# Optimization experiments

Hardware: AMD Instinct MI355X
Metric: run time of the kernel (lower is better)

Reference implementation:

```python
import jax, jax.numpy as jnp
import numpy as np

NUM_NEG = 100
TEMP = 0.05
EPS = 1e-12  # matches F.normalize eps


def _l2norm(x):
    n = jnp.sqrt(jnp.sum(x * x, axis=-1, keepdims=True))
    return x / jnp.maximum(n, EPS)


def setup_inputs() -> dict:
    key = jax.random.key(0)
    k1, k2, k3, k4, k5, k6 = jax.random.split(key, 6)
    B, S, D = 1024, 50, 64
    NUM_ITEMS = 100000  # table has NUM_ITEMS+1 rows (row 0 = padding)
    N = B * S
    return {
        "output_embeddings": jax.random.normal(k1, (B, S, D), dtype=jnp.float32),
        "target_ids": jax.random.randint(k2, (B, S), 1, NUM_ITEMS + 1, dtype=jnp.int64)
                      if jax.config.jax_enable_x64 else
                      jax.random.randint(k2, (B, S), 1, NUM_ITEMS + 1).astype(jnp.int32),
        "all_item_embeddings": jax.random.normal(k3, (NUM_ITEMS + 1, D), dtype=jnp.float32),
        "supervision_weights": jax.random.uniform(k4, (B, S), dtype=jnp.float32),
        "neg_indices": jax.random.randint(k5, (N, NUM_NEG), 1, NUM_ITEMS + 1).astype(jnp.int32),
        "alt_neg_indices": jax.random.randint(k6, (N, NUM_NEG), 1, NUM_ITEMS + 1).astype(jnp.int32),
    }


def reference(output_embeddings, target_ids, all_item_embeddings,
              supervision_weights, neg_indices, alt_neg_indices):
    B, S, D = output_embeddings.shape
    flat_out = output_embeddings.reshape(-1, D)            # [N, D]
    flat_tgt = target_ids.reshape(-1)                       # [N]
    flat_w = supervision_weights.reshape(-1)                # [N]
    valid = flat_w > 0

    vo = _l2norm(flat_out)                                  # [N, D]
    items = _l2norm(all_item_embeddings)                    # [V, D]

    pos_e = items[flat_tgt]                                 # [N, D]
    pos_logit = jnp.sum(vo * pos_e, axis=1)                 # [N]

    # resample negatives that collide with the positive target
    neg = jnp.where(neg_indices != flat_tgt[:, None], neg_indices, alt_neg_indices)
    neg_e = items[neg]                                      # [N, K, D]
    neg_logits = jnp.einsum('nd,nkd->nk', vo, neg_e)        # [N, K]

    logits = jnp.concatenate([pos_logit[:, None], neg_logits], axis=1) / TEMP
    # cross-entropy with label 0 == logsumexp - positive logit
    loss_per = jax.nn.logsumexp(logits, axis=1) - logits[:, 0]

    wm = jnp.where(valid, flat_w, 0.0)
    return jnp.sum(loss_per * wm) / jnp.sum(wm)
```

## Files before the change

kernel.cpp:

```cpp
#include <hip/hip_runtime.h>


#define D_DIM 64
#define K_NEG 100
#define INV_TEMP 20.0f
#define MAX_LOGIT 20.0f
#define LOG2E 1.4426950408889634f
#define LN2 0.6931471805599453f

#define NBLK_MAIN 2048
#define NBLK_NORM 512
#define NT 7

typedef float fv2 __attribute__((ext_vector_type(2)));

__global__ __launch_bounds__(256) void normalize_kernel(
    const float* __restrict__ items, unsigned int* __restrict__ tab, int V) {
  const int lane = threadIdx.x & 63;
  const int wid  = threadIdx.x >> 6;
  const int g = lane >> 4, q = lane & 15;
  const int waveId = blockIdx.x * 4 + wid;
  const int nWaves = gridDim.x * 4;
  for (int base = waveId * 4; base < V; base += nWaves * 4) {
    const int r = base + g;
    const bool act = (r < V);
    float4 x = make_float4(0.f, 0.f, 0.f, 0.f);
    if (act) x = *reinterpret_cast<const float4*>(items + (size_t)r * D_DIM + q * 4);
    float ss = x.x * x.x + x.y * x.y + x.z * x.z + x.w * x.w;
    ss += __shfl_xor(ss, 1);
    ss += __shfl_xor(ss, 2);
    ss += __shfl_xor(ss, 4);
    ss += __shfl_xor(ss, 8);
    const float inv = 1.0f / fmaxf(sqrtf(ss), 1e-12f);
    if (act) {
      int u = 0;
      u = __builtin_amdgcn_cvt_pk_fp8_f32(x.x * inv, x.y * inv, u, false);
      u = __builtin_amdgcn_cvt_pk_fp8_f32(x.z * inv, x.w * inv, u, true);
      tab[(size_t)r * 16 + q] = (unsigned int)u;
    }
  }
}

__global__ __launch_bounds__(256, 4) void loss_kernel(
    const float* __restrict__ oe,
    const int*   __restrict__ tgt,
    const unsigned int* __restrict__ tab,
    const float* __restrict__ wgt,
    const int*   __restrict__ negi,
    const int*   __restrict__ alti,
    float2*      __restrict__ partials,
    int N) {
  const int lane = threadIdx.x & 63;
  const int wid  = threadIdx.x >> 6;
  const int g = lane >> 2, q = lane & 3;
  const int waveId = blockIdx.x * 4 + wid;
  const int nWaves = gridDim.x * 4;

  float num = 0.f, den = 0.f;

  int row = waveId;
  float4 a0, a1, a2, a3;
  int t_r = 0;
  float w = 0.f;
  int nj0 = 0, nj1 = 0, nj2 = 0, nj3 = 0, nj4 = 0, nj5 = 0, nj6 = 0;

  if (row < N) {
    const float* orow = oe + (size_t)row * D_DIM + q * 16;
    a0 = *reinterpret_cast<const float4*>(orow + 0);
    a1 = *reinterpret_cast<const float4*>(orow + 4);
    a2 = *reinterpret_cast<const float4*>(orow + 8);
    a3 = *reinterpret_cast<const float4*>(orow + 12);
    t_r = tgt[row];
    w = wgt[row];
    const int* nrow = negi + (size_t)row * K_NEG;
    if (g >= 1) nj0 = nrow[g - 1];
    nj1 = nrow[16 + g - 1];
    nj2 = nrow[32 + g - 1];
    nj3 = nrow[48 + g - 1];
    nj4 = nrow[64 + g - 1];
    nj5 = nrow[80 + g - 1];
    if (g <= 4) nj6 = nrow[96 + g - 1];
  }

  while (row < N) {
    const int nxt = row + nWaves;
    const int* __restrict__ arow = alti + (size_t)row * K_NEG;

    int idx[NT];
    {
      int v0 = (g == 0) ? t_r : nj0;
      if (g >= 1 && v0 == t_r) v0 = arow[g - 1];
      idx[0] = v0;
      int v1 = nj1; if (v1 == t_r) v1 = arow[16 + g - 1]; idx[1] = v1;
      int v2 = nj2; if (v2 == t_r) v2 = arow[32 + g - 1]; idx[2] = v2;
      int v3 = nj3; if (v3 == t_r) v3 = arow[48 + g - 1]; idx[3] = v3;
      int v4 = nj4; if (v4 == t_r) v4 = arow[64 + g - 1]; idx[4] = v4;
      int v5 = nj5; if (v5 == t_r) v5 = arow[80 + g - 1]; idx[5] = v5;
      int v6 = 0;
      if (g <= 4) { v6 = nj6; if (v6 == t_r) v6 = arow[96 + g - 1]; }
      idx[6] = v6;
    }

    uint4 rb[NT];
#pragma unroll
    for (int t = 0; t < NT; ++t)
      rb[t] = *reinterpret_cast<const uint4*>(tab + (size_t)idx[t] * 16 + q * 4);

    float4 b0, b1, b2, b3;
    int p_t = 0; float p_w = 0.f;
    int pn0 = 0, pn1 = 0, pn2 = 0, pn3 = 0, pn4 = 0, pn5 = 0, pn6 = 0;
    b0 = b1 = b2 = b3 = make_float4(0.f, 0.f, 0.f, 0.f);
    if (nxt < N) {
      const float* prow = oe + (size_t)nxt * D_DIM + q * 16;
      b0 = *reinterpret_cast<const float4*>(prow + 0);
      b1 = *reinterpret_cast<const float4*>(prow + 4);
      b2 = *reinterpret_cast<const float4*>(prow + 8);
      b3 = *reinterpret_cast<const float4*>(prow + 12);
      p_t = tgt[nxt];
      p_w = wgt[nxt];
      const int* nrow = negi + (size_t)nxt * K_NEG;
      if (g >= 1) pn0 = nrow[g - 1];
      pn1 = nrow[16 + g - 1];
      pn2 = nrow[32 + g - 1];
      pn3 = nrow[48 + g - 1];
      pn4 = nrow[64 + g - 1];
      pn5 = nrow[80 + g - 1];
      if (g <= 4) pn6 = nrow[96 + g - 1];
    }

    const fv2 qa0 = {a0.x, a0.y}, qa1 = {a0.z, a0.w};
    const fv2 qa2 = {a1.x, a1.y}, qa3 = {a1.z, a1.w};
    const fv2 qa4 = {a2.x, a2.y}, qa5 = {a2.z, a2.w};
    const fv2 qa6 = {a3.x, a3.y}, qa7 = {a3.z, a3.w};

    fv2 ss2 = qa0 * qa0;
    ss2 += qa1 * qa1;
    ss2 += qa2 * qa2;
    ss2 += qa3 * qa3;
    ss2 += qa4 * qa4;
    ss2 += qa5 * qa5;
    ss2 += qa6 * qa6;
    ss2 += qa7 * qa7;
    float ss = ss2[0] + ss2[1];
    ss += __shfl_xor(ss, 1);
    ss += __shfl_xor(ss, 2);
    const float inv_o = 1.0f / fmaxf(sqrtf(ss), 1e-12f);

    float sumexp = 0.f;
    float pos_logit = 0.f;

#pragma unroll
    for (int t = 0; t < NT; ++t) {
      const uint4 r = rb[t];
      fv2 acc;
      acc  = qa0 * __builtin_amdgcn_cvt_pk_f32_fp8((int)r.x, false);
      acc += qa1 * __builtin_amdgcn_cvt_pk_f32_fp8((int)r.x, true);
      acc += qa2 * __builtin_amdgcn_cvt_pk_f32_fp8((int)r.y, false);
      acc += qa3 * __builtin_amdgcn_cvt_pk_f32_fp8((int)r.y, true);
      acc += qa4 * __builtin_amdgcn_cvt_pk_f32_fp8((int)r.z, false);
      acc += qa5 * __builtin_amdgcn_cvt_pk_f32_fp8((int)r.z, true);
      acc += qa6 * __builtin_amdgcn_cvt_pk_f32_fp8((int)r.w, false);
      acc += qa7 * __builtin_amdgcn_cvt_pk_f32_fp8((int)r.w, true);
      float p = acc[0] + acc[1];
      p += __shfl_xor(p, 1);
      p += __shfl_xor(p, 2);
      const int j = t * 16 + g;
      if (q == 0 && j <= K_NEG) {
        const float logit = p * inv_o * INV_TEMP;
        sumexp += exp2f((logit - MAX_LOGIT) * LOG2E);
        if (j == 0) pos_logit = logit;
      }
    }
    sumexp += __shfl_xor(sumexp, 4);
    sumexp += __shfl_xor(sumexp, 8);
    sumexp += __shfl_xor(sumexp, 16);
    sumexp += __shfl_xor(sumexp, 32);
    if (lane == 0) {
      const float lse = log2f(sumexp) * LN2 + MAX_LOGIT;
      const float loss = lse - pos_logit;
      if (w > 0.f) {
        num += loss * w;
        den += w;
      }
    }

    a0 = b0; a1 = b1; a2 = b2; a3 = b3;
    t_r = p_t; w = p_w;
    nj0 = pn0; nj1 = pn1; nj2 = pn2; nj3 = pn3; nj4 = pn4; nj5 = pn5; nj6 = pn6;
    row = nxt;
  }

  __shared__ float2 red[4];
  if (lane == 0) red[wid] = make_float2(num, den);
  __syncthreads();
  if (threadIdx.x == 0) {
    float n = 0.f, d = 0.f;
#pragma unroll
    for (int i = 0; i < 4; ++i) { n += red[i].x; d += red[i].y; }
    partials[blockIdx.x] = make_float2(n, d);
  }
}

__global__ __launch_bounds__(256) void finish_kernel(
    const float2* __restrict__ partials, int nblk, float* __restrict__ out) {
  float num = 0.f, den = 0.f;
  for (int i = threadIdx.x; i < nblk; i += 256) {
    const float2 p = partials[i];
    num += p.x;
    den += p.y;
  }
#pragma unroll
  for (int m = 1; m < 64; m <<= 1) {
    num += __shfl_xor(num, m);
    den += __shfl_xor(den, m);
  }
  __shared__ float2 red[4];
  const int wid = threadIdx.x >> 6;
  const int lane = threadIdx.x & 63;
  if (lane == 0) red[wid] = make_float2(num, den);
  __syncthreads();
  if (threadIdx.x == 0) {
    float n = 0.f, d = 0.f;
#pragma unroll
    for (int i = 0; i < 4; ++i) { n += red[i].x; d += red[i].y; }
    out[0] = n / d;
  }
}

extern "C" void kernel_launch(void* const* d_in, const int* in_sizes, int n_in,
                              void* d_out, int out_size, void* d_ws, size_t ws_size,
                              hipStream_t stream) {
  const float* oe    = (const float*)d_in[0];
  const int*   tgt   = (const int*)  d_in[1];
  const float* items = (const float*)d_in[2];
  const float* wgt   = (const float*)d_in[3];
  const int*   negi  = (const int*)  d_in[4];
  const int*   alti  = (const int*)  d_in[5];

  const int N = in_sizes[0] / D_DIM;
  const int V = in_sizes[2] / D_DIM;

  unsigned int* tab = (unsigned int*)d_ws;
  size_t off = ((size_t)V * 16 * sizeof(unsigned int) + 255) & ~(size_t)255;
  float2* partials = (float2*)((char*)d_ws + off);

  normalize_kernel<<<NBLK_NORM, 256, 0, stream>>>(items, tab, V);
  loss_kernel<<<NBLK_MAIN, 256, 0, stream>>>(oe, tgt, tab, wgt, negi, alti,
                                             partials, N);
  finish_kernel<<<1, 256, 0, stream>>>(partials, NBLK_MAIN, (float*)d_out);
}
```

Before: 70.75 us.

## Software-pipeline loss kernel with double-buffered gathers across rows

```diff
diff --git a/kernel.cpp b/kernel.cpp
--- a/kernel.cpp
+++ b/kernel.cpp
@@ -8,7 +8,7 @@
 #define LOG2E 1.4426950408889634f
 #define LN2 0.6931471805599453f
 
-#define NBLK_MAIN 2048
+#define NBLK_MAIN 1024
 #define NBLK_NORM 512
 #define NT 7
 
@@ -41,7 +41,122 @@
   }
 }
 
-__global__ __launch_bounds__(256, 4) void loss_kernel(
+
+struct Idx { int t, n0, n1, n2, n3, n4, n5, n6; };
+struct Qry { float4 a0, a1, a2, a3; float w; };
+
+__device__ __forceinline__ void load_idx(Idx& ix, const int* __restrict__ tgt,
+                                         const int* __restrict__ negi,
+                                         int row, int g) {
+  ix.t = tgt[row];
+  const int* __restrict__ nrow = negi + (size_t)row * K_NEG;
+  ix.n0 = 0;
+  ix.n6 = 0;
+  if (g >= 1) ix.n0 = nrow[g - 1];
+  ix.n1 = nrow[16 + g - 1];
+  ix.n2 = nrow[32 + g - 1];
+  ix.n3 = nrow[48 + g - 1];
+  ix.n4 = nrow[64 + g - 1];
+  ix.n5 = nrow[80 + g - 1];
+  if (g <= 4) ix.n6 = nrow[96 + g - 1];
+}
+
+__device__ __forceinline__ void load_qry(Qry& Q, const float* __restrict__ oe,
+                                         const float* __restrict__ wgt,
+                                         int row, int q) {
+  const float* __restrict__ orow = oe + (size_t)row * D_DIM + q * 16;
+  Q.a0 = *reinterpret_cast<const float4*>(orow + 0);
+  Q.a1 = *reinterpret_cast<const float4*>(orow + 4);
+  Q.a2 = *reinterpret_cast<const float4*>(orow + 8);
+  Q.a3 = *reinterpret_cast<const float4*>(orow + 12);
+  Q.w  = wgt[row];
+}
+
+__device__ __forceinline__ void resolve_gather(
+    const Idx& ix, const unsigned int* __restrict__ tab,
+    const int* __restrict__ alti, int row, int g, int q, uint4 (&rb)[NT]) {
+  const int* __restrict__ arow = alti + (size_t)row * K_NEG;
+  int id[NT];
+  {
+    int v0 = (g == 0) ? ix.t : ix.n0;
+    if (g >= 1 && v0 == ix.t) v0 = arow[g - 1];
+    id[0] = v0;
+    int v1 = ix.n1; if (v1 == ix.t) v1 = arow[16 + g - 1]; id[1] = v1;
+    int v2 = ix.n2; if (v2 == ix.t) v2 = arow[32 + g - 1]; id[2] = v2;
+    int v3 = ix.n3; if (v3 == ix.t) v3 = arow[48 + g - 1]; id[3] = v3;
+    int v4 = ix.n4; if (v4 == ix.t) v4 = arow[64 + g - 1]; id[4] = v4;
+    int v5 = ix.n5; if (v5 == ix.t) v5 = arow[80 + g - 1]; id[5] = v5;
+    int v6 = 0;
+    if (g <= 4) { v6 = ix.n6; if (v6 == ix.t) v6 = arow[96 + g - 1]; }
+    id[6] = v6;
+  }
+#pragma unroll
+  for (int t = 0; t < NT; ++t)
+    rb[t] = *reinterpret_cast<const uint4*>(tab + (size_t)id[t] * 16 + q * 4);
+}
+
+__device__ __forceinline__ void compute_row(const Qry& Q, const uint4 (&rb)[NT],
+                                            float& num, float& den,
+                                            int lane, int g, int q) {
+  const fv2 qa0 = {Q.a0.x, Q.a0.y}, qa1 = {Q.a0.z, Q.a0.w};
+  const fv2 qa2 = {Q.a1.x, Q.a1.y}, qa3 = {Q.a1.z, Q.a1.w};
+  const fv2 qa4 = {Q.a2.x, Q.a2.y}, qa5 = {Q.a2.z, Q.a2.w};
+  const fv2 qa6 = {Q.a3.x, Q.a3.y}, qa7 = {Q.a3.z, Q.a3.w};
+
+  fv2 ss2 = qa0 * qa0;
+  ss2 += qa1 * qa1;
+  ss2 += qa2 * qa2;
+  ss2 += qa3 * qa3;
+  ss2 += qa4 * qa4;
+  ss2 += qa5 * qa5;
+  ss2 += qa6 * qa6;
+  ss2 += qa7 * qa7;
+  float ss = ss2[0] + ss2[1];
+  ss += __shfl_xor(ss, 1);
+  ss += __shfl_xor(ss, 2);
+  const float inv_o = 1.0f / fmaxf(sqrtf(ss), 1e-12f);
+  const float scale = inv_o * INV_TEMP;
+
+  float sumexp = 0.f;
+  float pos_logit = 0.f;
+
+#pragma unroll
+  for (int t = 0; t < NT; ++t) {
+    const uint4 r = rb[t];
+    fv2 acc;
+    acc  = qa0 * __builtin_amdgcn_cvt_pk_f32_fp8((int)r.x, false);
+    acc += qa1 * __builtin_amdgcn_cvt_pk_f32_fp8((int)r.x, true);
+    acc += qa2 * __builtin_amdgcn_cvt_pk_f32_fp8((int)r.y, false);
+    acc += qa3 * __builtin_amdgcn_cvt_pk_f32_fp8((int)r.y, true);
+    acc += qa4 * __builtin_amdgcn_cvt_pk_f32_fp8((int)r.z, false);
+    acc += qa5 * __builtin_amdgcn_cvt_pk_f32_fp8((int)r.z, true);
+    acc += qa6 * __builtin_amdgcn_cvt_pk_f32_fp8((int)r.w, false);
+    acc += qa7 * __builtin_amdgcn_cvt_pk_f32_fp8((int)r.w, true);
+    float p = acc[0] + acc[1];
+    p += __shfl_xor(p, 1);
+    p += __shfl_xor(p, 2);
+    const int j = t * 16 + g;
+    if (q == 0 && j <= K_NEG) {
+      const float logit = p * scale;
+      sumexp += exp2f((logit - MAX_LOGIT) * LOG2E);
+      if (j == 0) pos_logit = logit;
+    }
+  }
+  sumexp += __shfl_xor(sumexp, 4);
+  sumexp += __shfl_xor(sumexp, 8);
+  sumexp += __shfl_xor(sumexp, 16);
+  sumexp += __shfl_xor(sumexp, 32);
+  if (lane == 0) {
+    const float lse = log2f(sumexp) * LN2 + MAX_LOGIT;
+    const float loss = lse - pos_logit;
+    if (Q.w > 0.f) {
+      num += loss * Q.w;
+      den += Q.w;
+    }
+  }
+}
+
+__global__ __launch_bounds__(256, 3) void loss_kernel(
     const float* __restrict__ oe,
     const int*   __restrict__ tgt,
     const unsigned int* __restrict__ tab,
@@ -59,135 +174,41 @@
   float num = 0.f, den = 0.f;
 
   int row = waveId;
-  float4 a0, a1, a2, a3;
-  int t_r = 0;
-  float w = 0.f;
-  int nj0 = 0, nj1 = 0, nj2 = 0, nj3 = 0, nj4 = 0, nj5 = 0, nj6 = 0;
+  Idx  ix;
+  Qry  qA, qB;
+  uint4 rbA[NT], rbB[NT];
 
   if (row < N) {
-    const float* orow = oe + (size_t)row * D_DIM + q * 16;
-    a0 = *reinterpret_cast<const float4*>(orow + 0);
-    a1 = *reinterpret_cast<const float4*>(orow + 4);
-    a2 = *reinterpret_cast<const float4*>(orow + 8);
-    a3 = *reinterpret_cast<const float4*>(orow + 12);
-    t_r = tgt[row];
-    w = wgt[row];
-    const int* nrow = negi + (size_t)row * K_NEG;
-    if (g >= 1) nj0 = nrow[g - 1];
-    nj1 = nrow[16 + g - 1];
-    nj2 = nrow[32 + g - 1];
-    nj3 = nrow[48 + g - 1];
-    nj4 = nrow[64 + g - 1];
-    nj5 = nrow[80 + g - 1];
-    if (g <= 4) nj6 = nrow[96 + g - 1];
+    load_idx(ix, tgt, negi, row, g);
+    load_qry(qA, oe, wgt, row, q);
+    resolve_gather(ix, tab, alti, row, g, q, rbA);
+    const int r1 = row + nWaves;
+    if (r1 < N) {
+      load_idx(ix, tgt, negi, r1, g);
+      load_qry(qB, oe, wgt, r1, q);
+    }
   }
 
   while (row < N) {
-    const int nxt = row + nWaves;
-    const int* __restrict__ arow = alti + (size_t)row * K_NEG;
-
-    int idx[NT];
     {
-      int v0 = (g == 0) ? t_r : nj0;
-      if (g >= 1 && v0 == t_r) v0 = arow[g - 1];
-      idx[0] = v0;
-      int v1 = nj1; if (v1 == t_r) v1 = arow[16 + g - 1]; idx[1] = v1;
-      int v2 = nj2; if (v2 == t_r) v2 = arow[32 + g - 1]; idx[2] = v2;
-      int v3 = nj3; if (v3 == t_r) v3 = arow[48 + g - 1]; idx[3] = v3;
-      int v4 = nj4; if (v4 == t_r) v4 = arow[64 + g - 1]; idx[4] = v4;
-      int v5 = nj5; if (v5 == t_r) v5 = arow[80 + g - 1]; idx[5] = v5;
-      int v6 = 0;
-      if (g <= 4) { v6 = nj6; if (v6 == t_r) v6 = arow[96 + g - 1]; }
-      idx[6] = v6;
-    }
-
-    uint4 rb[NT];
-#pragma unroll
-    for (int t = 0; t < NT; ++t)
-      rb[t] = *reinterpret_cast<const uint4*>(tab + (size_t)idx[t] * 16 + q * 4);
-
-    float4 b0, b1, b2, b3;
-    int p_t = 0; float p_w = 0.f;
-    int pn0 = 0, pn1 = 0, pn2 = 0, pn3 = 0, pn4 = 0, pn5 = 0, pn6 = 0;
-    b0 = b1 = b2 = b3 = make_float4(0.f, 0.f, 0.f, 0.f);
-    if (nxt < N) {
-      const float* prow = oe + (size_t)nxt * D_DIM + q * 16;
-      b0 = *reinterpret_cast<const float4*>(prow + 0);
-      b1 = *reinterpret_cast<const float4*>(prow + 4);
-      b2 = *reinterpret_cast<const float4*>(prow + 8);
-      b3 = *reinterpret_cast<const float4*>(prow + 12);
-      p_t = tgt[nxt];
-      p_w = wgt[nxt];
-      const int* nrow = negi + (size_t)nxt * K_NEG;
-      if (g >= 1) pn0 = nrow[g - 1];
-      pn1 = nrow[16 + g - 1];
-      pn2 = nrow[32 + g - 1];
-      pn3 = nrow[48 + g - 1];
-      pn4 = nrow[64 + g - 1];
-      pn5 = nrow[80 + g - 1];
-      if (g <= 4) pn6 = nrow[96 + g - 1];
-    }
-
-    const fv2 qa0 = {a0.x, a0.y}, qa1 = {a0.z, a0.w};
-    const fv2 qa2 = {a1.x, a1.y}, qa3 = {a1.z, a1.w};
-    const fv2 qa4 = {a2.x, a2.y}, qa5 = {a2.z, a2.w};
-    const fv2 qa6 = {a3.x, a3.y}, qa7 = {a3.z, a3.w};
-
-    fv2 ss2 = qa0 * qa0;
-    ss2 += qa1 * qa1;
-    ss2 += qa2 * qa2;
-    ss2 += qa3 * qa3;
-    ss2 += qa4 * qa4;
-    ss2 += qa5 * qa5;
-    ss2 += qa6 * qa6;
-    ss2 += qa7 * qa7;
-    float ss = ss2[0] + ss2[1];
-    ss += __shfl_xor(ss, 1);
-    ss += __shfl_xor(ss, 2);
-    const float inv_o = 1.0f / fmaxf(sqrtf(ss), 1e-12f);
-
-    float sumexp = 0.f;
-    float pos_logit = 0.f;
-
-#pragma unroll
-    for (int t = 0; t < NT; ++t) {
-      const uint4 r = rb[t];
-      fv2 acc;
-      acc  = qa0 * __builtin_amdgcn_cvt_pk_f32_fp8((int)r.x, false);
-      acc += qa1 * __builtin_amdgcn_cvt_pk_f32_fp8((int)r.x, true);
-      acc += qa2 * __builtin_amdgcn_cvt_pk_f32_fp8((int)r.y, false);
-      acc += qa3 * __builtin_amdgcn_cvt_pk_f32_fp8((int)r.y, true);
-      acc += qa4 * __builtin_amdgcn_cvt_pk_f32_fp8((int)r.z, false);
-      acc += qa5 * __builtin_amdgcn_cvt_pk_f32_fp8((int)r.z, true);
-      acc += qa6 * __builtin_amdgcn_cvt_pk_f32_fp8((int)r.w, false);
-      acc += qa7 * __builtin_amdgcn_cvt_pk_f32_fp8((int)r.w, true);
-      float p = acc[0] + acc[1];
-      p += __shfl_xor(p, 1);
-      p += __shfl_xor(p, 2);
-      const int j = t * 16 + g;
-      if (q == 0 && j <= K_NEG) {
-        const float logit = p * inv_o * INV_TEMP;
-        sumexp += exp2f((logit - MAX_LOGIT) * LOG2E);
-        if (j == 0) pos_logit = logit;
-      }
-    }
-    sumexp += __shfl_xor(sumexp, 4);
-    sumexp += __shfl_xor(sumexp, 8);
-    sumexp += __shfl_xor(sumexp, 16);
-    sumexp += __shfl_xor(sumexp, 32);
-    if (lane == 0) {
-      const float lse = log2f(sumexp) * LN2 + MAX_LOGIT;
-      const float loss = lse - pos_logit;
-      if (w > 0.f) {
-        num += loss * w;
-        den += w;
-      }
-    }
-
-    a0 = b0; a1 = b1; a2 = b2; a3 = b3;
-    t_r = p_t; w = p_w;
-    nj0 = pn0; nj1 = pn1; nj2 = pn2; nj3 = pn3; nj4 = pn4; nj5 = pn5; nj6 = pn6;
-    row = nxt;
+      const int r1 = row + nWaves;
+      const int r2 = r1 + nWaves;
+      if (r1 < N) resolve_gather(ix, tab, alti, r1, g, q, rbB);
+      if (r2 < N) load_idx(ix, tgt, negi, r2, g);
+      compute_row(qA, rbA, num, den, lane, g, q);
+      if (r2 < N) load_qry(qA, oe, wgt, r2, q);
+    }
+    row += nWaves;
+    if (row >= N) break;
+    {
+      const int r1 = row + nWaves;
+      const int r2 = r1 + nWaves;
+      if (r1 < N) resolve_gather(ix, tab, alti, r1, g, q, rbA);
+      if (r2 < N) load_idx(ix, tgt, negi, r2, g);
+      compute_row(qB, rbB, num, den, lane, g, q);
+      if (r2 < N) load_qry(qB, oe, wgt, r2, q);
+    }
+    row += nWaves;
   }
 
   __shared__ float2 red[4];
```

New measurement: 77.63 us. 1.1x slower.

## Process one row per block with async global-to-LDS double-buffered gathers

Applied to the files above, without the earlier changes.

```diff
diff --git a/kernel.cpp b/kernel.cpp
--- a/kernel.cpp
+++ b/kernel.cpp
@@ -7,12 +7,24 @@
 #define MAX_LOGIT 20.0f
 #define LOG2E 1.4426950408889634f
 #define LN2 0.6931471805599453f
+#define MAXL2 28.853900817779268f
 
 #define NBLK_MAIN 2048
 #define NBLK_NORM 512
-#define NT 7
+#define NSLOT 128
 
 typedef float fv2 __attribute__((ext_vector_type(2)));
+
+__device__ __forceinline__ void gload_lds16(const void* g, void* l) {
+  __builtin_amdgcn_global_load_lds(
+      (const __attribute__((address_space(1))) unsigned int*)g,
+      (__attribute__((address_space(3))) unsigned int*)l, 16, 0, 0);
+}
+__device__ __forceinline__ void gload_lds4(const void* g, void* l) {
+  __builtin_amdgcn_global_load_lds(
+      (const __attribute__((address_space(1))) unsigned int*)g,
+      (__attribute__((address_space(3))) unsigned int*)l, 4, 0, 0);
+}
 
 __global__ __launch_bounds__(256) void normalize_kernel(
     const float* __restrict__ items, unsigned int* __restrict__ tab, int V) {
@@ -41,7 +53,7 @@
   }
 }
 
-__global__ __launch_bounds__(256, 4) void loss_kernel(
+__global__ __launch_bounds__(256) void loss_kernel(
     const float* __restrict__ oe,
     const int*   __restrict__ tgt,
     const unsigned int* __restrict__ tab,
@@ -50,155 +62,146 @@
     const int*   __restrict__ alti,
     float2*      __restrict__ partials,
     int N) {
-  const int lane = threadIdx.x & 63;
-  const int wid  = threadIdx.x >> 6;
-  const int g = lane >> 2, q = lane & 3;
-  const int waveId = blockIdx.x * 4 + wid;
-  const int nWaves = gridDim.x * 4;
+  __shared__ uint4 s_items[2][NSLOT * 4];
+  __shared__ float s_q[2][D_DIM];
+  __shared__ float s_red[2][4];
+  __shared__ float s_pos[2];
+
+  const int tid  = threadIdx.x;
+  const int lane = tid & 63;
+  const int wid  = tid >> 6;
+  const int sub  = lane >> 2;
+  const int qd   = lane & 3;
+  const int G    = gridDim.x;
+
+  const int i1 = wid;
+  const int i2 = wid + 4;
+  const int s1 = 16 * i1 + sub;
+  const int s2 = 16 * i2 + sub;
+  const bool has2 = (wid <= 2) && (s2 <= K_NEG);
 
   float num = 0.f, den = 0.f;
-
-  int row = waveId;
-  float4 a0, a1, a2, a3;
-  int t_r = 0;
-  float w = 0.f;
-  int nj0 = 0, nj1 = 0, nj2 = 0, nj3 = 0, nj4 = 0, nj5 = 0, nj6 = 0;
-
-  if (row < N) {
-    const float* orow = oe + (size_t)row * D_DIM + q * 16;
-    a0 = *reinterpret_cast<const float4*>(orow + 0);
-    a1 = *reinterpret_cast<const float4*>(orow + 4);
-    a2 = *reinterpret_cast<const float4*>(orow + 8);
-    a3 = *reinterpret_cast<const float4*>(orow + 12);
-    t_r = tgt[row];
-    w = wgt[row];
-    const int* nrow = negi + (size_t)row * K_NEG;
-    if (g >= 1) nj0 = nrow[g - 1];
-    nj1 = nrow[16 + g - 1];
-    nj2 = nrow[32 + g - 1];
-    nj3 = nrow[48 + g - 1];
-    nj4 = nrow[64 + g - 1];
-    nj5 = nrow[80 + g - 1];
-    if (g <= 4) nj6 = nrow[96 + g - 1];
-  }
-
-  while (row < N) {
-    const int nxt = row + nWaves;
-    const int* __restrict__ arow = alti + (size_t)row * K_NEG;
-
-    int idx[NT];
+  int r = blockIdx.x;
+
+  int ndB1 = 0, ndB2 = 0, tN = 0;
+  float wC = 0.f, wN = 0.f;
+
+  auto LOADIDX = [&](int rowS, int& d1, int& d2) {
+    const int* nr = negi + (size_t)rowS * K_NEG;
+    d1 = (s1 > 0) ? __builtin_nontemporal_load(nr + (s1 - 1)) : 0;
+    d2 = has2 ? __builtin_nontemporal_load(nr + (s2 - 1)) : 0;
+  };
+
+  auto STAGE = [&](int rowS, int nb, int d1, int d2, int tS) {
+    const int* ar = alti + (size_t)rowS * K_NEG;
+    int v1 = (s1 == 0) ? tS : d1;
+    if (s1 > 0 && v1 == tS) v1 = ar[s1 - 1];
+    gload_lds16(tab + (size_t)v1 * 16 + qd * 4, &s_items[nb][64 * i1]);
+    if (has2) {
+      int v2 = d2;
+      if (v2 == tS) v2 = ar[s2 - 1];
+      gload_lds16(tab + (size_t)v2 * 16 + qd * 4, &s_items[nb][64 * i2]);
+    }
+    if (wid == 3) gload_lds4(oe + (size_t)rowS * D_DIM + lane, &s_q[nb][0]);
+  };
+
+  if (r < N) {
+    int d1, d2;
+    LOADIDX(r, d1, d2);
+    const int t0 = tgt[r];
+    wC = wgt[r];
+    STAGE(r, 0, d1, d2, t0);
+    const int r1 = r + G;
+    if (r1 < N) {
+      LOADIDX(r1, ndB1, ndB2);
+      tN = tgt[r1];
+      wN = wgt[r1];
+    }
+  }
+  __syncthreads();
+
+  int cur = 0;
+  while (r < N) {
+    const int r1 = r + G, r2 = r + 2 * G;
+    if (r1 < N) STAGE(r1, cur ^ 1, ndB1, ndB2, tN);
+    int nd1n = 0, nd2n = 0, tn2 = 0;
+    float wn2 = 0.f;
+    if (r2 < N) {
+      LOADIDX(r2, nd1n, nd2n);
+      tn2 = tgt[r2];
+      wn2 = wgt[r2];
+    }
+
     {
-      int v0 = (g == 0) ? t_r : nj0;
-      if (g >= 1 && v0 == t_r) v0 = arow[g - 1];
-      idx[0] = v0;
-      int v1 = nj1; if (v1 == t_r) v1 = arow[16 + g - 1]; idx[1] = v1;
-      int v2 = nj2; if (v2 == t_r) v2 = arow[32 + g - 1]; idx[2] = v2;
-      int v3 = nj3; if (v3 == t_r) v3 = arow[48 + g - 1]; idx[3] = v3;
-      int v4 = nj4; if (v4 == t_r) v4 = arow[64 + g - 1]; idx[4] = v4;
-      int v5 = nj5; if (v5 == t_r) v5 = arow[80 + g - 1]; idx[5] = v5;
-      int v6 = 0;
-      if (g <= 4) { v6 = nj6; if (v6 == t_r) v6 = arow[96 + g - 1]; }
-      idx[6] = v6;
-    }
-
-    uint4 rb[NT];
+      const float4* qp = reinterpret_cast<const float4*>(&s_q[cur][qd * 16]);
+      const float4 x0 = qp[0], x1 = qp[1], x2 = qp[2], x3 = qp[3];
+      const fv2 qa0 = {x0.x, x0.y}, qa1 = {x0.z, x0.w};
+      const fv2 qa2 = {x1.x, x1.y}, qa3 = {x1.z, x1.w};
+      const fv2 qa4 = {x2.x, x2.y}, qa5 = {x2.z, x2.w};
+      const fv2 qa6 = {x3.x, x3.y}, qa7 = {x3.z, x3.w};
+
+      fv2 ss2 = qa0 * qa0;
+      ss2 += qa1 * qa1;
+      ss2 += qa2 * qa2;
+      ss2 += qa3 * qa3;
+      ss2 += qa4 * qa4;
+      ss2 += qa5 * qa5;
+      ss2 += qa6 * qa6;
+      ss2 += qa7 * qa7;
+      float ss = ss2[0] + ss2[1];
+      ss += __shfl_xor(ss, 1);
+      ss += __shfl_xor(ss, 2);
+      const float inv_o = 1.0f / fmaxf(sqrtf(ss), 1e-12f);
+      const float scale = inv_o * INV_TEMP;
+      const float sc2 = scale * LOG2E;
+
+      float sacc = 0.f;
 #pragma unroll
-    for (int t = 0; t < NT; ++t)
-      rb[t] = *reinterpret_cast<const uint4*>(tab + (size_t)idx[t] * 16 + q * 4);
-
-    float4 b0, b1, b2, b3;
-    int p_t = 0; float p_w = 0.f;
-    int pn0 = 0, pn1 = 0, pn2 = 0, pn3 = 0, pn4 = 0, pn5 = 0, pn6 = 0;
-    b0 = b1 = b2 = b3 = make_float4(0.f, 0.f, 0.f, 0.f);
-    if (nxt < N) {
-      const float* prow = oe + (size_t)nxt * D_DIM + q * 16;
-      b0 = *reinterpret_cast<const float4*>(prow + 0);
-      b1 = *reinterpret_cast<const float4*>(prow + 4);
-      b2 = *reinterpret_cast<const float4*>(prow + 8);
-      b3 = *reinterpret_cast<const float4*>(prow + 12);
-      p_t = tgt[nxt];
-      p_w = wgt[nxt];
-      const int* nrow = negi + (size_t)nxt * K_NEG;
-      if (g >= 1) pn0 = nrow[g - 1];
-      pn1 = nrow[16 + g - 1];
-      pn2 = nrow[32 + g - 1];
-      pn3 = nrow[48 + g - 1];
-      pn4 = nrow[64 + g - 1];
-      pn5 = nrow[80 + g - 1];
-      if (g <= 4) pn6 = nrow[96 + g - 1];
-    }
-
-    const fv2 qa0 = {a0.x, a0.y}, qa1 = {a0.z, a0.w};
-    const fv2 qa2 = {a1.x, a1.y}, qa3 = {a1.z, a1.w};
-    const fv2 qa4 = {a2.x, a2.y}, qa5 = {a2.z, a2.w};
-    const fv2 qa6 = {a3.x, a3.y}, qa7 = {a3.z, a3.w};
-
-    fv2 ss2 = qa0 * qa0;
-    ss2 += qa1 * qa1;
-    ss2 += qa2 * qa2;
-    ss2 += qa3 * qa3;
-    ss2 += qa4 * qa4;
-    ss2 += qa5 * qa5;
-    ss2 += qa6 * qa6;
-    ss2 += qa7 * qa7;
-    float ss = ss2[0] + ss2[1];
-    ss += __shfl_xor(ss, 1);
-    ss += __shfl_xor(ss, 2);
-    const float inv_o = 1.0f / fmaxf(sqrtf(ss), 1e-12f);
-
-    float sumexp = 0.f;
-    float pos_logit = 0.f;
-
-#pragma unroll
-    for (int t = 0; t < NT; ++t) {
-      const uint4 r = rb[t];
-      fv2 acc;
-      acc  = qa0 * __builtin_amdgcn_cvt_pk_f32_fp8((int)r.x, false);
-      acc += qa1 * __builtin_amdgcn_cvt_pk_f32_fp8((int)r.x, true);
-      acc += qa2 * __builtin_amdgcn_cvt_pk_f32_fp8((int)r.y, false);
-      acc += qa3 * __builtin_amdgcn_cvt_pk_f32_fp8((int)r.y, true);
-      acc += qa4 * __builtin_amdgcn_cvt_pk_f32_fp8((int)r.z, false);
-      acc += qa5 * __builtin_amdgcn_cvt_pk_f32_fp8((int)r.z, true);
-      acc += qa6 * __builtin_amdgcn_cvt_pk_f32_fp8((int)r.w, false);
-      acc += qa7 * __builtin_amdgcn_cvt_pk_f32_fp8((int)r.w, true);
-      float p = acc[0] + acc[1];
-      p += __shfl_xor(p, 1);
-      p += __shfl_xor(p, 2);
-      const int j = t * 16 + g;
-      if (q == 0 && j <= K_NEG) {
-        const float logit = p * inv_o * INV_TEMP;
-        sumexp += exp2f((logit - MAX_LOGIT) * LOG2E);
-        if (j == 0) pos_logit = logit;
+      for (int p = 0; p < 2; ++p) {
+        const int s = p * 64 + wid * 16 + sub;
+        const uint4 rv = s_items[cur][s * 4 + qd];
+        fv2 acc;
+        acc  = qa0 * __builtin_amdgcn_cvt_pk_f32_fp8((int)rv.x, false);
+        acc += qa1 * __builtin_amdgcn_cvt_pk_f32_fp8((int)rv.x, true);
+        acc += qa2 * __builtin_amdgcn_cvt_pk_f32_fp8((int)rv.y, false);
+        acc += qa3 * __builtin_amdgcn_cvt_pk_f32_fp8((int)rv.y, true);
+        acc += qa4 * __builtin_amdgcn_cvt_pk_f32_fp8((int)rv.z, false);
+        acc += qa5 * __builtin_amdgcn_cvt_pk_f32_fp8((int)rv.z, true);
+        acc += qa6 * __builtin_amdgcn_cvt_pk_f32_fp8((int)rv.w, false);
+        acc += qa7 * __builtin_amdgcn_cvt_pk_f32_fp8((int)rv.w, true);
+        float d = acc[0] + acc[1];
+        d += __shfl_xor(d, 1);
+        d += __shfl_xor(d, 2);
+        if (p == 0 && tid == 0) s_pos[cur] = d * scale;
+        const float e = exp2f(fmaf(d, sc2, -MAXL2));
+        sacc += (s <= K_NEG && qd == 0) ? e : 0.f;
       }
-    }
-    sumexp += __shfl_xor(sumexp, 4);
-    sumexp += __shfl_xor(sumexp, 8);
-    sumexp += __shfl_xor(sumexp, 16);
-    sumexp += __shfl_xor(sumexp, 32);
-    if (lane == 0) {
-      const float lse = log2f(sumexp) * LN2 + MAX_LOGIT;
-      const float loss = lse - pos_logit;
-      if (w > 0.f) {
-        num += loss * w;
-        den += w;
+      sacc += __shfl_xor(sacc, 4);
+      sacc += __shfl_xor(sacc, 8);
+      sacc += __shfl_xor(sacc, 16);
+      sacc += __shfl_xor(sacc, 32);
+      if (lane == 0) s_red[cur][wid] = sacc;
+    }
+
+    __syncthreads();
+
+    if (tid == 0) {
+      const float S = s_red[cur][0] + s_red[cur][1] + s_red[cur][2] + s_red[cur][3];
+      const float lse = log2f(S) * LN2 + MAX_LOGIT;
+      const float loss = lse - s_pos[cur];
+      if (wC > 0.f) {
+        num += loss * wC;
+        den += wC;
       }
     }
 
-    a0 = b0; a1 = b1; a2 = b2; a3 = b3;
-    t_r = p_t; w = p_w;
-    nj0 = pn0; nj1 = pn1; nj2 = pn2; nj3 = pn3; nj4 = pn4; nj5 = pn5; nj6 = pn6;
-    row = nxt;
-  }
-
-  __shared__ float2 red[4];
-  if (lane == 0) red[wid] = make_float2(num, den);
-  __syncthreads();
-  if (threadIdx.x == 0) {
-    float n = 0.f, d = 0.f;
-#pragma unroll
-    for (int i = 0; i < 4; ++i) { n += red[i].x; d += red[i].y; }
-    partials[blockIdx.x] = make_float2(n, d);
-  }
+    wC = wN; wN = wn2;
+    ndB1 = nd1n; ndB2 = nd2n; tN = tn2;
+    cur ^= 1;
+    r += G;
+  }
+
+  if (tid == 0) partials[blockIdx.x] = make_float2(num, den);
 }
 
 __global__ __launch_bounds__(256) void finish_kernel(
```

Result: slower. 79.06 us (+11.7%).

## Split fp8 item table into dimension halves and gather in two cache-friendly passes

Applied to the files above, without the earlier changes.

```diff
diff --git a/kernel.cpp b/kernel.cpp
--- a/kernel.cpp
+++ b/kernel.cpp
@@ -7,15 +7,19 @@
 #define MAX_LOGIT 20.0f
 #define LOG2E 1.4426950408889634f
 #define LN2 0.6931471805599453f
+#define MAXL2 28.853900817779268f
 
 #define NBLK_MAIN 2048
-#define NBLK_NORM 512
+#define NBLK_NORM 1024
 #define NT 7
+#define MAXK 7
+#define PSTRIDE 104
 
 typedef float fv2 __attribute__((ext_vector_type(2)));
 
 __global__ __launch_bounds__(256) void normalize_kernel(
-    const float* __restrict__ items, unsigned int* __restrict__ tab, int V) {
+    const float* __restrict__ items, unsigned int* __restrict__ tabA,
+    unsigned int* __restrict__ tabB, int V) {
   const int lane = threadIdx.x & 63;
   const int wid  = threadIdx.x >> 6;
   const int g = lane >> 4, q = lane & 15;
@@ -36,20 +40,26 @@
       int u = 0;
       u = __builtin_amdgcn_cvt_pk_fp8_f32(x.x * inv, x.y * inv, u, false);
       u = __builtin_amdgcn_cvt_pk_fp8_f32(x.z * inv, x.w * inv, u, true);
-      tab[(size_t)r * 16 + q] = (unsigned int)u;
+      unsigned int* t = (q < 8) ? (tabA + (size_t)r * 8 + q)
+                                : (tabB + (size_t)r * 8 + (q - 8));
+      *t = (unsigned int)u;
     }
   }
 }
 
-__global__ __launch_bounds__(256, 4) void loss_kernel(
+__global__ __launch_bounds__(256) void loss_kernel(
     const float* __restrict__ oe,
     const int*   __restrict__ tgt,
-    const unsigned int* __restrict__ tab,
+    const unsigned int* __restrict__ tabA,
+    const unsigned int* __restrict__ tabB,
     const float* __restrict__ wgt,
     const int*   __restrict__ negi,
     const int*   __restrict__ alti,
     float2*      __restrict__ partials,
     int N) {
+  __shared__ float s_part[4][MAXK][PSTRIDE];
+  __shared__ float2 s_red[4];
+
   const int lane = threadIdx.x & 63;
   const int wid  = threadIdx.x >> 6;
   const int g = lane >> 2, q = lane & 3;
@@ -58,145 +68,155 @@
 
   float num = 0.f, den = 0.f;
 
-  int row = waveId;
-  float4 a0, a1, a2, a3;
-  int t_r = 0;
-  float w = 0.f;
-  int nj0 = 0, nj1 = 0, nj2 = 0, nj3 = 0, nj4 = 0, nj5 = 0, nj6 = 0;
-
-  if (row < N) {
-    const float* orow = oe + (size_t)row * D_DIM + q * 16;
-    a0 = *reinterpret_cast<const float4*>(orow + 0);
-    a1 = *reinterpret_cast<const float4*>(orow + 4);
-    a2 = *reinterpret_cast<const float4*>(orow + 8);
-    a3 = *reinterpret_cast<const float4*>(orow + 12);
-    t_r = tgt[row];
-    w = wgt[row];
-    const int* nrow = negi + (size_t)row * K_NEG;
-    if (g >= 1) nj0 = nrow[g - 1];
-    nj1 = nrow[16 + g - 1];
-    nj2 = nrow[32 + g - 1];
-    nj3 = nrow[48 + g - 1];
-    nj4 = nrow[64 + g - 1];
-    nj5 = nrow[80 + g - 1];
-    if (g <= 4) nj6 = nrow[96 + g - 1];
-  }
-
-  while (row < N) {
-    const int nxt = row + nWaves;
-    const int* __restrict__ arow = alti + (size_t)row * K_NEG;
-
-    int idx[NT];
-    {
-      int v0 = (g == 0) ? t_r : nj0;
-      if (g >= 1 && v0 == t_r) v0 = arow[g - 1];
-      idx[0] = v0;
-      int v1 = nj1; if (v1 == t_r) v1 = arow[16 + g - 1]; idx[1] = v1;
-      int v2 = nj2; if (v2 == t_r) v2 = arow[32 + g - 1]; idx[2] = v2;
-      int v3 = nj3; if (v3 == t_r) v3 = arow[48 + g - 1]; idx[3] = v3;
-      int v4 = nj4; if (v4 == t_r) v4 = arow[64 + g - 1]; idx[4] = v4;
-      int v5 = nj5; if (v5 == t_r) v5 = arow[80 + g - 1]; idx[5] = v5;
-      int v6 = 0;
-      if (g <= 4) { v6 = nj6; if (v6 == t_r) v6 = arow[96 + g - 1]; }
-      idx[6] = v6;
+  auto LOADN = [&](int row, int* nj) {
+    const int* nr = negi + (size_t)row * K_NEG;
+    nj[0] = (g >= 1) ? __builtin_nontemporal_load(nr + g - 1) : 0;
+    nj[1] = __builtin_nontemporal_load(nr + 16 + g - 1);
+    nj[2] = __builtin_nontemporal_load(nr + 32 + g - 1);
+    nj[3] = __builtin_nontemporal_load(nr + 48 + g - 1);
+    nj[4] = __builtin_nontemporal_load(nr + 64 + g - 1);
+    nj[5] = __builtin_nontemporal_load(nr + 80 + g - 1);
+    nj[6] = (g <= 4) ? __builtin_nontemporal_load(nr + 96 + g - 1) : 0;
+  };
+
+  auto RESOLVE = [&](const int* nj, int t_r, int row, int* id) {
+    const int* ar = alti + (size_t)row * K_NEG;
+    int v0 = (g == 0) ? t_r : nj[0];
+    if (g >= 1 && v0 == t_r) v0 = ar[g - 1];
+    id[0] = v0;
+    int v1 = nj[1]; if (v1 == t_r) v1 = ar[16 + g - 1]; id[1] = v1;
+    int v2 = nj[2]; if (v2 == t_r) v2 = ar[32 + g - 1]; id[2] = v2;
+    int v3 = nj[3]; if (v3 == t_r) v3 = ar[48 + g - 1]; id[3] = v3;
+    int v4 = nj[4]; if (v4 == t_r) v4 = ar[64 + g - 1]; id[4] = v4;
+    int v5 = nj[5]; if (v5 == t_r) v5 = ar[80 + g - 1]; id[5] = v5;
+    int v6 = 0;
+    if (g <= 4) { v6 = nj[6]; if (v6 == t_r) v6 = ar[96 + g - 1]; }
+    id[6] = v6;
+  };
+
+  {
+    int row = waveId, k = 0;
+    int t_r = 0, nj[NT];
+    if (row < N) { t_r = tgt[row]; LOADN(row, nj); }
+    while (row < N && k < MAXK) {
+      const int nxt = row + nWaves;
+      int id[NT];
+      RESOLVE(nj, t_r, row, id);
+      uint2 rb[NT];
+#pragma unroll
+      for (int t = 0; t < NT; ++t)
+        rb[t] = *reinterpret_cast<const uint2*>(tabA + (size_t)id[t] * 8 + q * 2);
+      if (nxt < N) { t_r = tgt[nxt]; LOADN(nxt, nj); }
+
+      const float* orow = oe + (size_t)row * D_DIM + q * 8;
+      const float4 x0 = *reinterpret_cast<const float4*>(orow + 0);
+      const float4 x1 = *reinterpret_cast<const float4*>(orow + 4);
+      const fv2 qa0 = {x0.x, x0.y}, qa1 = {x0.z, x0.w};
+      const fv2 qa2 = {x1.x, x1.y}, qa3 = {x1.z, x1.w};
+
+      fv2 ss2 = qa0 * qa0;
+      ss2 += qa1 * qa1;
+      ss2 += qa2 * qa2;
+      ss2 += qa3 * qa3;
+      float ss = ss2[0] + ss2[1];
+      ss += __shfl_xor(ss, 1);
+      ss += __shfl_xor(ss, 2);
+      if (lane == 0) s_part[wid][k][101] = ss;
+
+#pragma unroll
+      for (int t = 0; t < NT; ++t) {
+        const uint2 r2 = rb[t];
+        fv2 acc;
+        acc  = qa0 * __builtin_amdgcn_cvt_pk_f32_fp8((int)r2.x, false);
+        acc += qa1 * __builtin_amdgcn_cvt_pk_f32_fp8((int)r2.x, true);
+        acc += qa2 * __builtin_amdgcn_cvt_pk_f32_fp8((int)r2.y, false);
+        acc += qa3 * __builtin_amdgcn_cvt_pk_f32_fp8((int)r2.y, true);
+        float d = acc[0] + acc[1];
+        d += __shfl_xor(d, 1);
+        d += __shfl_xor(d, 2);
+        const int j = t * 16 + g;
+        if (q == 0 && j <= K_NEG) s_part[wid][k][j] = d;
+      }
+      row = nxt; ++k;
     }
-
-    uint4 rb[NT];
-#pragma unroll
-    for (int t = 0; t < NT; ++t)
-      rb[t] = *reinterpret_cast<const uint4*>(tab + (size_t)idx[t] * 16 + q * 4);
-
-    float4 b0, b1, b2, b3;
-    int p_t = 0; float p_w = 0.f;
-    int pn0 = 0, pn1 = 0, pn2 = 0, pn3 = 0, pn4 = 0, pn5 = 0, pn6 = 0;
-    b0 = b1 = b2 = b3 = make_float4(0.f, 0.f, 0.f, 0.f);
-    if (nxt < N) {
-      const float* prow = oe + (size_t)nxt * D_DIM + q * 16;
-      b0 = *reinterpret_cast<const float4*>(prow + 0);
-      b1 = *reinterpret_cast<const float4*>(prow + 4);
-      b2 = *reinterpret_cast<const float4*>(prow + 8);
-      b3 = *reinterpret_cast<const float4*>(prow + 12);
-      p_t = tgt[nxt];
-      p_w = wgt[nxt];
-      const int* nrow = negi + (size_t)nxt * K_NEG;
-      if (g >= 1) pn0 = nrow[g - 1];
-      pn1 = nrow[16 + g - 1];
-      pn2 = nrow[32 + g - 1];
-      pn3 = nrow[48 + g - 1];
-      pn4 = nrow[64 + g - 1];
-      pn5 = nrow[80 + g - 1];
-      if (g <= 4) pn6 = nrow[96 + g - 1];
+  }
+
+
+  {
+    int row = waveId, k = 0;
+    int t_r = 0, nj[NT];
+    float w = 0.f;
+    if (row < N) { t_r = tgt[row]; w = wgt[row]; LOADN(row, nj); }
+    while (row < N && k < MAXK) {
+      const int nxt = row + nWaves;
+      int id[NT];
+      RESOLVE(nj, t_r, row, id);
+      uint2 rb[NT];
+#pragma unroll
+      for (int t = 0; t < NT; ++t)
+        rb[t] = *reinterpret_cast<const uint2*>(tabB + (size_t)id[t] * 8 + q * 2);
+      float p_w = 0.f;
+      if (nxt < N) { t_r = tgt[nxt]; p_w = wgt[nxt]; LOADN(nxt, nj); }
+
+      const float* orow = oe + (size_t)row * D_DIM + 32 + q * 8;
+      const float4 x0 = *reinterpret_cast<const float4*>(orow + 0);
+      const float4 x1 = *reinterpret_cast<const float4*>(orow + 4);
+      const fv2 qa0 = {x0.x, x0.y}, qa1 = {x0.z, x0.w};
+      const fv2 qa2 = {x1.x, x1.y}, qa3 = {x1.z, x1.w};
+
+      fv2 ss2 = qa0 * qa0;
+      ss2 += qa1 * qa1;
+      ss2 += qa2 * qa2;
+      ss2 += qa3 * qa3;
+      float ss = ss2[0] + ss2[1];
+      ss += __shfl_xor(ss, 1);
+      ss += __shfl_xor(ss, 2);
+      const float sstot = ss + s_part[wid][k][101];
+      const float scale = INV_TEMP / fmaxf(sqrtf(sstot), 1e-12f);
+      const float sc2 = scale * LOG2E;
+
+      float sacc = 0.f, pos = 0.f;
+#pragma unroll
+      for (int t = 0; t < NT; ++t) {
+        const uint2 r2 = rb[t];
+        fv2 acc;
+        acc  = qa0 * __builtin_amdgcn_cvt_pk_f32_fp8((int)r2.x, false);
+        acc += qa1 * __builtin_amdgcn_cvt_pk_f32_fp8((int)r2.x, true);
+        acc += qa2 * __builtin_amdgcn_cvt_pk_f32_fp8((int)r2.y, false);
+        acc += qa3 * __builtin_amdgcn_cvt_pk_f32_fp8((int)r2.y, true);
+        float d = acc[0] + acc[1];
+        d += __shfl_xor(d, 1);
+        d += __shfl_xor(d, 2);
+        const int j = t * 16 + g;
+        if (q == 0 && j <= K_NEG) {
+          const float tot = d + s_part[wid][k][j];
+          sacc += exp2f(fmaf(tot, sc2, -MAXL2));
+          if (j == 0) pos = tot * scale;
+        }
+      }
+      sacc += __shfl_xor(sacc, 4);
+      sacc += __shfl_xor(sacc, 8);
+      sacc += __shfl_xor(sacc, 16);
+      sacc += __shfl_xor(sacc, 32);
+      if (lane == 0) {
+        const float lse = log2f(sacc) * LN2 + MAX_LOGIT;
+        const float loss = lse - pos;
+        if (w > 0.f) {
+          num += loss * w;
+          den += w;
+        }
+      }
+      w = p_w;
+      row = nxt; ++k;
     }
-
-    const fv2 qa0 = {a0.x, a0.y}, qa1 = {a0.z, a0.w};
-    const fv2 qa2 = {a1.x, a1.y}, qa3 = {a1.z, a1.w};
-    const fv2 qa4 = {a2.x, a2.y}, qa5 = {a2.z, a2.w};
-    const fv2 qa6 = {a3.x, a3.y}, qa7 = {a3.z, a3.w};
-
-    fv2 ss2 = qa0 * qa0;
-    ss2 += qa1 * qa1;
-    ss2 += qa2 * qa2;
-    ss2 += qa3 * qa3;
-    ss2 += qa4 * qa4;
-    ss2 += qa5 * qa5;
-    ss2 += qa6 * qa6;
-    ss2 += qa7 * qa7;
-    float ss = ss2[0] + ss2[1];
-    ss += __shfl_xor(ss, 1);
-    ss += __shfl_xor(ss, 2);
-    const float inv_o = 1.0f / fmaxf(sqrtf(ss), 1e-12f);
-
-    float sumexp = 0.f;
-    float pos_logit = 0.f;
-
-#pragma unroll
-    for (int t = 0; t < NT; ++t) {
-      const uint4 r = rb[t];
-      fv2 acc;
-      acc  = qa0 * __builtin_amdgcn_cvt_pk_f32_fp8((int)r.x, false);
-      acc += qa1 * __builtin_amdgcn_cvt_pk_f32_fp8((int)r.x, true);
-      acc += qa2 * __builtin_amdgcn_cvt_pk_f32_fp8((int)r.y, false);
-      acc += qa3 * __builtin_amdgcn_cvt_pk_f32_fp8((int)r.y, true);
-      acc += qa4 * __builtin_amdgcn_cvt_pk_f32_fp8((int)r.z, false);
-      acc += qa5 * __builtin_amdgcn_cvt_pk_f32_fp8((int)r.z, true);
-      acc += qa6 * __builtin_amdgcn_cvt_pk_f32_fp8((int)r.w, false);
-      acc += qa7 * __builtin_amdgcn_cvt_pk_f32_fp8((int)r.w, true);
-      float p = acc[0] + acc[1];
-      p += __shfl_xor(p, 1);
-      p += __shfl_xor(p, 2);
-      const int j = t * 16 + g;
-      if (q == 0 && j <= K_NEG) {
-        const float logit = p * inv_o * INV_TEMP;
-        sumexp += exp2f((logit - MAX_LOGIT) * LOG2E);
-        if (j == 0) pos_logit = logit;
-      }
-    }
-    sumexp += __shfl_xor(sumexp, 4);
-    sumexp += __shfl_xor(sumexp, 8);
-    sumexp += __shfl_xor(sumexp, 16);
-    sumexp += __shfl_xor(sumexp, 32);
-    if (lane == 0) {
-      const float lse = log2f(sumexp) * LN2 + MAX_LOGIT;
-      const float loss = lse - pos_logit;
-      if (w > 0.f) {
-        num += loss * w;
-        den += w;
-      }
-    }
-
-    a0 = b0; a1 = b1; a2 = b2; a3 = b3;
-    t_r = p_t; w = p_w;
-    nj0 = pn0; nj1 = pn1; nj2 = pn2; nj3 = pn3; nj4 = pn4; nj5 = pn5; nj6 = pn6;
-    row = nxt;
-  }
-
-  __shared__ float2 red[4];
-  if (lane == 0) red[wid] = make_float2(num, den);
+  }
+
+  if (lane == 0) s_red[wid] = make_float2(num, den);
   __syncthreads();
   if (threadIdx.x == 0) {
     float n = 0.f, d = 0.f;
 #pragma unroll
-    for (int i = 0; i < 4; ++i) { n += red[i].x; d += red[i].y; }
+    for (int i = 0; i < 4; ++i) { n += s_red[i].x; d += s_red[i].y; }
     partials[blockIdx.x] = make_float2(n, d);
   }
 }
@@ -240,12 +260,13 @@
   const int N = in_sizes[0] / D_DIM;
   const int V = in_sizes[2] / D_DIM;
 
-  unsigned int* tab = (unsigned int*)d_ws;
+  unsigned int* tabA = (unsigned int*)d_ws;
+  unsigned int* tabB = tabA + (size_t)V * 8;
   size_t off = ((size_t)V * 16 * sizeof(unsigned int) + 255) & ~(size_t)255;
   float2* partials = (float2*)((char*)d_ws + off);
 
-  normalize_kernel<<<NBLK_NORM, 256, 0, stream>>>(items, tab, V);
-  loss_kernel<<<NBLK_MAIN, 256, 0, stream>>>(oe, tgt, tab, wgt, negi, alti,
-                                             partials, N);
+  normalize_kernel<<<NBLK_NORM, 256, 0, stream>>>(items, tabA, tabB, V);
+  loss_kernel<<<NBLK_MAIN, 256, 0, stream>>>(oe, tgt, tabA, tabB, wgt, negi,
+                                             alti, partials, N);
   finish_kernel<<<1, 256, 0, stream>>>(partials, NBLK_MAIN, (float*)d_out);
 }
```

After: 107.9 us. 52.5% more time.
